# Kernel tuning notes

Hardware: AMD Instinct MI355X
Metric: run time of the kernel (lower is better)

The kernel has to match this reference:

```python
import jax, jax.numpy as jnp
import numpy as np

INPUT_DIM = 1024
UNITS = 1024

def setup_inputs() -> dict:
    key = jax.random.key(0)
    ks = jax.random.split(key, 7)
    B, S = 4, 2048
    x = jax.random.normal(ks[0], (B, S, INPUT_DIM), dtype=jnp.float32)
    # nn.Linear weights stored as [out, in]; biases [out]
    scale = 1.0 / np.sqrt(INPUT_DIM)
    Wq = jax.random.uniform(ks[1], (UNITS, INPUT_DIM), jnp.float32, -scale, scale)
    bq = jax.random.uniform(ks[2], (UNITS,), jnp.float32, -scale, scale)
    Wk = jax.random.uniform(ks[3], (UNITS, INPUT_DIM), jnp.float32, -scale, scale)
    bk = jax.random.uniform(ks[4], (UNITS,), jnp.float32, -scale, scale)
    Wv = jax.random.uniform(ks[5], (UNITS, INPUT_DIM), jnp.float32, -scale, scale)
    bv = jax.random.uniform(ks[6], (UNITS,), jnp.float32, -scale, scale)
    return {"x": x, "Wq": Wq, "bq": bq, "Wk": Wk, "bk": bk, "Wv": Wv, "bv": bv}

def reference(x, Wq, bq, Wk, bk, Wv, bv):
    # Q/K/V projections: [B,S,D] @ [D,U]
    Q = jnp.einsum('bsd,ud->bsu', x, Wq) + bq
    K = jnp.einsum('bsd,ud->bsu', x, Wk) + bk
    V = jnp.einsum('bsd,ud->bsu', x, Wv) + bv
    scores = jnp.einsum('bqu,bku->bqk', Q, K) / jnp.sqrt(jnp.float32(UNITS))
    attn = jax.nn.softmax(scores, axis=-1)
    return jnp.einsum('bqk,bku->bqu', attn, V)
```

## Files before the change

kernel.cpp:

```cpp
#include <hip/hip_runtime.h>
#include <cstdint>
#include <cstddef>


typedef unsigned short ushort_t;
typedef __attribute__((ext_vector_type(8))) short short8;
typedef __attribute__((ext_vector_type(4))) float f32x4;

#define AS1 __attribute__((address_space(1)))
#define AS3 __attribute__((address_space(3)))

__device__ __forceinline__ ushort_t f2bf(float f) {
    unsigned int u = __float_as_uint(f);
    u += 0x7FFFu + ((u >> 16) & 1u);
    return (ushort_t)(u >> 16);
}
__device__ __forceinline__ float bf2f(ushort_t b) {
    return __uint_as_float(((unsigned)b) << 16);
}

__device__ __forceinline__ void async_ld16(const void* g, unsigned lds_off) {
    __builtin_amdgcn_global_load_lds((const AS1 void*)(uintptr_t)g,
                                     (AS3 void*)(uintptr_t)lds_off,
                                     16, 0, 0);
}

template <typename OT, int EPI, int NB, int BK>
__global__ __launch_bounds__(256, 2) void gemm_bt(
    const ushort_t* __restrict__ A, const ushort_t* __restrict__ B0,
    const ushort_t* __restrict__ B1,
    const float* __restrict__ bias0, const float* __restrict__ bias1,
    OT* __restrict__ C0, OT* __restrict__ C1,
    int K, int lda, int ldb, int ldc, float scale,
    long long aOffZ, long long bOffZ, long long cOffZ, long long biasOffZ)
{
    constexpr int P     = BK / 8;
    constexpr int NCALL = BK / 16;
    constexpr int RPC   = 2048 / BK;

    __shared__ __align__(16) ushort_t As[128 * BK];
    __shared__ __align__(16) ushort_t Bs[NB][128 * BK];

    const int tid  = threadIdx.x;
    const int wave = tid >> 6;
    const int lane = tid & 63;

    A  += (size_t)blockIdx.z * aOffZ;
    B0 += (size_t)blockIdx.z * bOffZ;
    if (NB == 2) B1 += (size_t)blockIdx.z * bOffZ;
    bias0 += (size_t)blockIdx.z * biasOffZ;

    const int m0 = blockIdx.y * 128;
    const int n0 = blockIdx.x * 128;
    const int wm = (wave >> 1) * 64;
    const int wn = (wave & 1) * 64;

    const unsigned ldsA  = (unsigned)(uintptr_t)&As[0];
    const unsigned ldsB0 = (unsigned)(uintptr_t)&Bs[0][0];
    const unsigned ldsB1 = (NB == 2) ? (unsigned)(uintptr_t)&Bs[NB - 1][0] : 0;

    const int srow = wave * (RPC / 4) + lane / P;
    const int cd   = ((lane & (P - 1)) - srow) & (P - 1);
    const ushort_t* gA  = A  + (size_t)(m0 + srow) * lda + cd * 8;
    const ushort_t* gB0 = B0 + (size_t)(n0 + srow) * ldb + cd * 8;
    const ushort_t* gB1 = (NB == 2) ? B1 + (size_t)(n0 + srow) * ldb + cd * 8
                                    : nullptr;
    const unsigned lw = (wave << 10);

    const int frow = lane & 15;
    const int fg   = lane >> 4;

    f32x4 acc[NB][4][4] = {};

    for (int k0 = 0; k0 < K; k0 += BK) {
        if (k0) __syncthreads();
#pragma unroll
        for (int c = 0; c < NCALL; ++c) {
            const size_t ro = (size_t)c * RPC;
            async_ld16(gA + ro * lda, ldsA + c * 4096 + lw);
            async_ld16(gB0 + ro * ldb, ldsB0 + c * 4096 + lw);
            if (NB == 2) async_ld16(gB1 + ro * ldb, ldsB1 + c * 4096 + lw);
        }
        gA += BK; gB0 += BK; if (NB == 2) gB1 += BK;
        __syncthreads();

#pragma unroll
        for (int t = 0; t < BK / 32; ++t) {
            const int pa = (((t << 2) + fg + frow) & (P - 1)) << 3;
            short8 af[4], bf[4];
#pragma unroll
            for (int i = 0; i < 4; ++i)
                af[i] = *(const short8*)&As[(wm + i * 16 + frow) * BK + pa];
#pragma unroll
            for (int j = 0; j < 4; ++j)
                bf[j] = *(const short8*)&Bs[0][(wn + j * 16 + frow) * BK + pa];
#pragma unroll
            for (int i = 0; i < 4; ++i)
#pragma unroll
                for (int j = 0; j < 4; ++j)
                    acc[0][i][j] = __builtin_amdgcn_mfma_f32_16x16x32_bf16(
                        af[i], bf[j], acc[0][i][j], 0, 0, 0);
            if (NB == 2) {
#pragma unroll
                for (int j = 0; j < 4; ++j)
                    bf[j] = *(const short8*)&Bs[NB - 1][(wn + j * 16 + frow) * BK + pa];
#pragma unroll
                for (int i = 0; i < 4; ++i)
#pragma unroll
                    for (int j = 0; j < 4; ++j)
                        acc[NB - 1][i][j] = __builtin_amdgcn_mfma_f32_16x16x32_bf16(
                            af[i], bf[j], acc[NB - 1][i][j], 0, 0, 0);
            }
        }
    }

    const int r0 = (lane >> 4) << 2;
    const int c0 = lane & 15;
#pragma unroll
    for (int o = 0; o < NB; ++o) {
        OT* C = (o == 0) ? C0 : C1;
        C += (size_t)blockIdx.z * cOffZ;
        const float* bia = (o == 0) ? bias0 : bias1;
#pragma unroll
        for (int i = 0; i < 4; ++i) {
            float bm[4];
            if (EPI == 2 || EPI == 4) {
#pragma unroll
                for (int r = 0; r < 4; ++r)
                    bm[r] = bias0[m0 + wm + i * 16 + r0 + r];
                if (EPI == 4) {
#pragma unroll
                    for (int r = 0; r < 4; ++r) bm[r] = 1.0f / bm[r];
                }
            }
#pragma unroll
            for (int j = 0; j < 4; ++j) {
                const int n = n0 + wn + j * 16 + c0;
                const float bn = (EPI == 1) ? bia[n] : 0.f;
#pragma unroll
                for (int r = 0; r < 4; ++r) {
                    const int m = m0 + wm + i * 16 + r0 + r;
                    float v = acc[o][i][j][r] * scale;
                    if (EPI == 1) v += bn;
                    if (EPI == 2) v += bm[r];
                    if (EPI == 3) v = __expf(v);
                    if (EPI == 4) v *= bm[r];
                    if constexpr (sizeof(OT) == 2)
                        C[(size_t)m * ldc + n] = f2bf(v);
                    else
                        C[(size_t)m * ldc + n] = v;
                }
            }
        }
    }
}

__global__ __launch_bounds__(256) void cvt_f32_bf16(
    const float* __restrict__ in, ushort_t* __restrict__ out, int n)
{
    const int i = (blockIdx.x * 256 + threadIdx.x) * 8;
    if (i >= n) return;
    const f32x4 a = *(const f32x4*)(in + i);
    const f32x4 b = *(const f32x4*)(in + i + 4);
    short8 o;
    o[0] = (short)f2bf(a[0]); o[1] = (short)f2bf(a[1]);
    o[2] = (short)f2bf(a[2]); o[3] = (short)f2bf(a[3]);
    o[4] = (short)f2bf(b[0]); o[5] = (short)f2bf(b[1]);
    o[6] = (short)f2bf(b[2]); o[7] = (short)f2bf(b[3]);
    *(short8*)(out + i) = o;
}

__global__ __launch_bounds__(256) void rowsum_rows(
    const ushort_t* __restrict__ S, float* __restrict__ rs)
{
    const int tid = threadIdx.x;
    const ushort_t* p = S + (size_t)blockIdx.x * 2048 + tid * 8;
    const short8 raw = *(const short8*)p;
    float s = 0.f;
#pragma unroll
    for (int j = 0; j < 8; ++j) s += bf2f((ushort_t)raw[j]);
#pragma unroll
    for (int off = 32; off > 0; off >>= 1) s += __shfl_xor(s, off, 64);
    __shared__ float red[4];
    const int wave = tid >> 6, lane = tid & 63;
    if (lane == 0) red[wave] = s;
    __syncthreads();
    if (tid == 0) rs[blockIdx.x] = (red[0] + red[1]) + (red[2] + red[3]);
}

extern "C" void kernel_launch(void* const* d_in, const int* in_sizes, int n_in,
                              void* d_out, int out_size, void* d_ws, size_t ws_size,
                              hipStream_t stream)
{
    const float* x  = (const float*)d_in[0];
    const float* Wq = (const float*)d_in[1];
    const float* bq = (const float*)d_in[2];
    const float* Wk = (const float*)d_in[3];
    const float* bk = (const float*)d_in[4];
    const float* Wv = (const float*)d_in[5];
    const float* bv = (const float*)d_in[6];
    float* out = (float*)d_out;

    char* ws = (char*)d_ws;
    const size_t MB = 1ull << 20;
    ushort_t* Xb  = (ushort_t*)(ws);
    ushort_t* Wqb = (ushort_t*)(ws + 16 * MB);
    ushort_t* Wkb = (ushort_t*)(ws + 18 * MB);
    ushort_t* Wvb = (ushort_t*)(ws + 20 * MB);
    ushort_t* Qb  = (ushort_t*)(ws + 32 * MB);
    ushort_t* Kb  = (ushort_t*)(ws + 48 * MB);
    ushort_t* Vt  = (ushort_t*)(ws + 64 * MB);
    ushort_t* Sc  = (ushort_t*)(ws);
    float*    Rs  = (float*)(ws + 32 * MB);

    cvt_f32_bf16<<<dim3(4096), dim3(256), 0, stream>>>(x, Xb, 8388608);
    cvt_f32_bf16<<<dim3(512), dim3(256), 0, stream>>>(Wq, Wqb, 1048576);
    cvt_f32_bf16<<<dim3(512), dim3(256), 0, stream>>>(Wk, Wkb, 1048576);
    cvt_f32_bf16<<<dim3(512), dim3(256), 0, stream>>>(Wv, Wvb, 1048576);

    gemm_bt<ushort_t, 1, 2, 64><<<dim3(8, 64, 1), dim3(256), 0, stream>>>(
        Xb, Wqb, Wkb, bq, bk, Qb, Kb, 1024, 1024, 1024, 1024, 1.0f,
        0, 0, 0, 0);

    gemm_bt<ushort_t, 2, 1, 64><<<dim3(64, 8, 1), dim3(256), 0, stream>>>(
        Wvb, Xb, nullptr, bv, nullptr, Vt, nullptr,
        1024, 1024, 1024, 8192, 1.0f, 0, 0, 0, 0);

    gemm_bt<ushort_t, 3, 1, 32><<<dim3(16, 16, 4), dim3(256), 0, stream>>>(
        Qb, Kb, nullptr, nullptr, nullptr, Sc, nullptr,
        1024, 1024, 1024, 2048, 0.03125f,
        2048ll * 1024, 2048ll * 1024, 2048ll * 2048, 0);

    rowsum_rows<<<dim3(8192), dim3(256), 0, stream>>>(Sc, Rs);

    gemm_bt<float, 4, 1, 64><<<dim3(8, 16, 4), dim3(256), 0, stream>>>(
        Sc, Vt, nullptr, Rs, nullptr, out, nullptr,
        2048, 2048, 8192, 1024, 1.0f,
        2048ll * 2048, 2048ll, 2048ll * 1024, 2048);
}
```

Measured before the change: 257.0 us.

## Fuse softmax row-sum into PV GEMM, merge conversion kernels, widen QK tile

Computes the softmax denominator inside the final attention-times-V GEMM by summing the bf16 score fragments already loaded into LDS, which removes the separate rowsum kernel and its full pass over the score matrix. The four fp32-to-bf16 conversion launches are merged into one kernel to cut launch overhead. The QK^T GEMM's K-tile is raised from 32 to 64. In exchange, the waves holding the left-half tile do extra scalar adds in the main loop, and the larger tile uses more LDS.

```diff
diff --git a/kernel.cpp b/kernel.cpp
--- a/kernel.cpp
+++ b/kernel.cpp
@@ -32,7 +32,7 @@
     const float* __restrict__ bias0, const float* __restrict__ bias1,
     OT* __restrict__ C0, OT* __restrict__ C1,
     int K, int lda, int ldb, int ldc, float scale,
-    long long aOffZ, long long bOffZ, long long cOffZ, long long biasOffZ)
+    long long aOffZ, long long bOffZ, long long cOffZ)
 {
     constexpr int P     = BK / 8;
     constexpr int NCALL = BK / 16;
@@ -40,6 +40,7 @@
 
     __shared__ __align__(16) ushort_t As[128 * BK];
     __shared__ __align__(16) ushort_t Bs[NB][128 * BK];
+    __shared__ float rs[128];
 
     const int tid  = threadIdx.x;
     const int wave = tid >> 6;
@@ -48,7 +49,6 @@
     A  += (size_t)blockIdx.z * aOffZ;
     B0 += (size_t)blockIdx.z * bOffZ;
     if (NB == 2) B1 += (size_t)blockIdx.z * bOffZ;
-    bias0 += (size_t)blockIdx.z * biasOffZ;
 
     const int m0 = blockIdx.y * 128;
     const int n0 = blockIdx.x * 128;
@@ -71,6 +71,7 @@
     const int fg   = lane >> 4;
 
     f32x4 acc[NB][4][4] = {};
+    float rsacc[4] = {0.f, 0.f, 0.f, 0.f};
 
     for (int k0 = 0; k0 < K; k0 += BK) {
         if (k0) __syncthreads();
@@ -91,6 +92,13 @@
 #pragma unroll
             for (int i = 0; i < 4; ++i)
                 af[i] = *(const short8*)&As[(wm + i * 16 + frow) * BK + pa];
+            if (EPI == 4 && wn == 0) {
+#pragma unroll
+                for (int i = 0; i < 4; ++i)
+#pragma unroll
+                    for (int e = 0; e < 8; ++e)
+                        rsacc[i] += bf2f((ushort_t)af[i][e]);
+            }
 #pragma unroll
             for (int j = 0; j < 4; ++j)
                 bf[j] = *(const short8*)&Bs[0][(wn + j * 16 + frow) * BK + pa];
@@ -114,6 +122,19 @@
         }
     }
 
+    if (EPI == 4) {
+        if (wn == 0) {
+#pragma unroll
+            for (int i = 0; i < 4; ++i) {
+                float s = rsacc[i];
+                s += __shfl_xor(s, 16, 64);
+                s += __shfl_xor(s, 32, 64);
+                rs[wm + i * 16 + frow] = s;
+            }
+        }
+        __syncthreads();
+    }
+
     const int r0 = (lane >> 4) << 2;
     const int c0 = lane & 15;
 #pragma unroll
@@ -124,14 +145,15 @@
 #pragma unroll
         for (int i = 0; i < 4; ++i) {
             float bm[4];
-            if (EPI == 2 || EPI == 4) {
+            if (EPI == 2) {
 #pragma unroll
                 for (int r = 0; r < 4; ++r)
                     bm[r] = bias0[m0 + wm + i * 16 + r0 + r];
-                if (EPI == 4) {
-#pragma unroll
-                    for (int r = 0; r < 4; ++r) bm[r] = 1.0f / bm[r];
-                }
+            }
+            if (EPI == 4) {
+#pragma unroll
+                for (int r = 0; r < 4; ++r)
+                    bm[r] = 1.0f / rs[wm + i * 16 + r0 + r];
             }
 #pragma unroll
             for (int j = 0; j < 4; ++j) {
@@ -155,37 +177,27 @@
     }
 }
 
-__global__ __launch_bounds__(256) void cvt_f32_bf16(
-    const float* __restrict__ in, ushort_t* __restrict__ out, int n)
+__global__ __launch_bounds__(256) void cvt_all(
+    const float* __restrict__ x,  const float* __restrict__ wq,
+    const float* __restrict__ wk, const float* __restrict__ wv,
+    ushort_t* __restrict__ xb,  ushort_t* __restrict__ wqb,
+    ushort_t* __restrict__ wkb, ushort_t* __restrict__ wvb)
 {
-    const int i = (blockIdx.x * 256 + threadIdx.x) * 8;
-    if (i >= n) return;
-    const f32x4 a = *(const f32x4*)(in + i);
-    const f32x4 b = *(const f32x4*)(in + i + 4);
+    const int b = blockIdx.x;
+    const float* src; ushort_t* dst; size_t base;
+    if (b < 4096)      { src = x;  dst = xb;  base = (size_t)b * 2048; }
+    else if (b < 4608) { src = wq; dst = wqb; base = (size_t)(b - 4096) * 2048; }
+    else if (b < 5120) { src = wk; dst = wkb; base = (size_t)(b - 4608) * 2048; }
+    else               { src = wv; dst = wvb; base = (size_t)(b - 5120) * 2048; }
+    const size_t i = base + threadIdx.x * 8;
+    const f32x4 a = *(const f32x4*)(src + i);
+    const f32x4 c = *(const f32x4*)(src + i + 4);
     short8 o;
     o[0] = (short)f2bf(a[0]); o[1] = (short)f2bf(a[1]);
     o[2] = (short)f2bf(a[2]); o[3] = (short)f2bf(a[3]);
-    o[4] = (short)f2bf(b[0]); o[5] = (short)f2bf(b[1]);
-    o[6] = (short)f2bf(b[2]); o[7] = (short)f2bf(b[3]);
-    *(short8*)(out + i) = o;
-}
-
-__global__ __launch_bounds__(256) void rowsum_rows(
-    const ushort_t* __restrict__ S, float* __restrict__ rs)
-{
-    const int tid = threadIdx.x;
-    const ushort_t* p = S + (size_t)blockIdx.x * 2048 + tid * 8;
-    const short8 raw = *(const short8*)p;
-    float s = 0.f;
-#pragma unroll
-    for (int j = 0; j < 8; ++j) s += bf2f((ushort_t)raw[j]);
-#pragma unroll
-    for (int off = 32; off > 0; off >>= 1) s += __shfl_xor(s, off, 64);
-    __shared__ float red[4];
-    const int wave = tid >> 6, lane = tid & 63;
-    if (lane == 0) red[wave] = s;
-    __syncthreads();
-    if (tid == 0) rs[blockIdx.x] = (red[0] + red[1]) + (red[2] + red[3]);
+    o[4] = (short)f2bf(c[0]); o[5] = (short)f2bf(c[1]);
+    o[6] = (short)f2bf(c[2]); o[7] = (short)f2bf(c[3]);
+    *(short8*)(dst + i) = o;
 }
 
 extern "C" void kernel_launch(void* const* d_in, const int* in_sizes, int n_in,
@@ -211,30 +223,24 @@
     ushort_t* Kb  = (ushort_t*)(ws + 48 * MB);
     ushort_t* Vt  = (ushort_t*)(ws + 64 * MB);
     ushort_t* Sc  = (ushort_t*)(ws);
-    float*    Rs  = (float*)(ws + 32 * MB);
-
-    cvt_f32_bf16<<<dim3(4096), dim3(256), 0, stream>>>(x, Xb, 8388608);
-    cvt_f32_bf16<<<dim3(512), dim3(256), 0, stream>>>(Wq, Wqb, 1048576);
-    cvt_f32_bf16<<<dim3(512), dim3(256), 0, stream>>>(Wk, Wkb, 1048576);
-    cvt_f32_bf16<<<dim3(512), dim3(256), 0, stream>>>(Wv, Wvb, 1048576);
+
+    cvt_all<<<dim3(5632), dim3(256), 0, stream>>>(
+        x, Wq, Wk, Wv, Xb, Wqb, Wkb, Wvb);
 
     gemm_bt<ushort_t, 1, 2, 64><<<dim3(8, 64, 1), dim3(256), 0, stream>>>(
-        Xb, Wqb, Wkb, bq, bk, Qb, Kb, 1024, 1024, 1024, 1024, 1.0f,
-        0, 0, 0, 0);
+        Xb, Wqb, Wkb, bq, bk, Qb, Kb, 1024, 1024, 1024, 1024, 1.0f, 0, 0, 0);
 
     gemm_bt<ushort_t, 2, 1, 64><<<dim3(64, 8, 1), dim3(256), 0, stream>>>(
         Wvb, Xb, nullptr, bv, nullptr, Vt, nullptr,
-        1024, 1024, 1024, 8192, 1.0f, 0, 0, 0, 0);
-
-    gemm_bt<ushort_t, 3, 1, 32><<<dim3(16, 16, 4), dim3(256), 0, stream>>>(
+        1024, 1024, 1024, 8192, 1.0f, 0, 0, 0);
+
+    gemm_bt<ushort_t, 3, 1, 64><<<dim3(16, 16, 4), dim3(256), 0, stream>>>(
         Qb, Kb, nullptr, nullptr, nullptr, Sc, nullptr,
         1024, 1024, 1024, 2048, 0.03125f,
-        2048ll * 1024, 2048ll * 1024, 2048ll * 2048, 0);
-
-    rowsum_rows<<<dim3(8192), dim3(256), 0, stream>>>(Sc, Rs);
+        2048ll * 1024, 2048ll * 1024, 2048ll * 2048);
 
     gemm_bt<float, 4, 1, 64><<<dim3(8, 16, 4), dim3(256), 0, stream>>>(
-        Sc, Vt, nullptr, Rs, nullptr, out, nullptr,
+        Sc, Vt, nullptr, nullptr, nullptr, out, nullptr,
         2048, 2048, 8192, 1024, 1.0f,
-        2048ll * 2048, 2048ll, 2048ll * 1024, 2048);
-}
+        2048ll * 2048, 2048ll, 2048ll * 1024);
+}
```

Result: faster. 249.9 us (-2.8%).
